# Kernel tuning notes

Hardware: AMD Instinct MI355X
Metric: run time of the kernel (lower is better)

## Reference

```python
import jax, jax.numpy as jnp
import numpy as np

N_DISEASES = 8192
N_MIRNAS = 16384
N_TOTAL = N_DISEASES + N_MIRNAS
D = 256
B = 65536
K = 50
EPS = 1e-8


def setup_inputs() -> dict:
    key = jax.random.key(0)
    k1, k2, k3, k4, k5, k6 = jax.random.split(key, 6)
    h = jax.random.normal(k1, (N_TOTAL, D), dtype=jnp.float32)
    emb = jax.random.normal(k2, (N_TOTAL, D), dtype=jnp.float32)
    src_init = jax.random.normal(k3, (B, D), dtype=jnp.float32)
    dst_init = jax.random.normal(k4, (B, D), dtype=jnp.float32)
    diseases = jax.random.randint(k5, (B,), 0, N_DISEASES, dtype=jnp.int32)
    mirnas = jax.random.randint(k6, (B,), N_DISEASES, N_TOTAL, dtype=jnp.int32)
    return {"h": h, "emb": emb, "src_init": src_init, "dst_init": dst_init,
            "diseases": diseases, "mirnas": mirnas}


def _cos(a, b):
    # cosine similarity along the last axis, eps-clamped like torch's F.cosine_similarity
    na = jnp.maximum(jnp.linalg.norm(a, axis=-1), EPS)
    nb = jnp.maximum(jnp.linalg.norm(b, axis=-1), EPS)
    return jnp.sum(a * b, axis=-1) / (na * nb)


def _pair_contrastive(pos_sim, neg_sim):
    # -log(exp(pos) / (exp(pos) + exp(neg))) = logaddexp(0, neg - pos)
    return jnp.mean(jnp.logaddexp(jnp.float32(0.0), neg_sim - pos_sim))


def _knn_feature_update(features, k):
    # [N, N] dense similarity, top-(k+1), drop self, gather + mean
    sim = features @ features.T                      # [N, N]
    _, idx = jax.lax.top_k(sim, k + 1)               # [N, k+1]
    idx = idx[:, 1:]                                 # drop self-match
    nbr = features[idx]                              # [N, k, D]
    return jnp.mean(nbr, axis=1)                     # [N, D]


def _knn_contrastive(feat_a, feat_b):
    center_a = jnp.mean(feat_a, axis=0)
    center_b = jnp.mean(feat_b, axis=0)
    sa_a = _cos(feat_a, center_a[None, :])
    sb_a = _cos(feat_a, center_b[None, :])
    loss_a = _pair_contrastive(sa_a, sb_a)
    sb_b = _cos(feat_b, center_b[None, :])
    sa_b = _cos(feat_b, center_a[None, :])
    loss_b = _pair_contrastive(sb_b, sa_b)
    return (loss_a + loss_b) * jnp.float32(0.5)


def reference(h, emb, src_init, dst_init, diseases, mirnas):
    h_d = h[diseases]                                # [B, D]
    h_m = h[mirnas]                                  # [B, D]
    pos_sim = _cos(h_d, src_init)
    neg_sim = _cos(h_d, dst_init)
    contrastive_loss = _pair_contrastive(pos_sim, neg_sim)

    upd_d = _knn_feature_update(emb[:N_DISEASES], K)
    upd_m = _knn_feature_update(emb[N_DISEASES:], K)
    feature_contrastive_loss = _knn_contrastive(upd_d, upd_m)

    # interactionPredictor modeled as sigmoid dot-product scorer
    scores = jax.nn.sigmoid(jnp.sum(h_d * h_m, axis=-1))  # [B]
    return scores, contrastive_loss, feature_contrastive_loss
```

## Files before the change

kernel.cpp:

```cpp
#include <hip/hip_runtime.h>
#include <math.h>

#define NDIS 8192
#define NMIR 16384
#define NTOT 24576
#define DIMD 256
#define BPAIR 65536
#define KSEL 50
#define EPSF 1e-8f
#define CBC 32
#define CAP 80
#define PSTR 320
#define ZD 2.066f
#define ZM 2.418f
#define ZFD 0.9035f
#define ZFM 1.331f
#define NKB 768

typedef __attribute__((ext_vector_type(8))) short bf16x8;
typedef __attribute__((ext_vector_type(4))) float f32x4;
typedef unsigned long long ull;

__device__ __forceinline__ float wredsum(float v) {
#pragma unroll
  for (int off = 1; off < 64; off <<= 1) v += __shfl_xor(v, off, 64);
  return v;
}

__device__ __forceinline__ int wredsumi(int v) {
#pragma unroll
  for (int off = 1; off < 64; off <<= 1) v += __shfl_xor(v, off, 64);
  return v;
}

__device__ __forceinline__ float softplusf(float x) {
  return fmaxf(x, 0.0f) + log1pf(expf(-fabsf(x)));
}

__device__ __forceinline__ float dot4f(const float4 a, const float4 b) {
  return a.x * b.x + a.y * b.y + a.z * b.z + a.w * b.w;
}

__device__ __forceinline__ unsigned short f2bf(float f) {
  unsigned u = __float_as_uint(f);
  unsigned r = (u + 0x7fffu + ((u >> 16) & 1u)) >> 16;
  return (unsigned short)r;
}

__device__ __forceinline__ float b2f(unsigned short x) {
  return __uint_as_float((unsigned)x << 16);
}

__device__ __forceinline__ unsigned ordu(float f) {
  unsigned u = __float_as_uint(f);
  return (u & 0x80000000u) ? ~u : (u | 0x80000000u);
}

__global__ __launch_bounds__(256) void convert_kernel(
    const float* __restrict__ in, unsigned short* __restrict__ out) {
  const int i = (blockIdx.x * 256 + threadIdx.x) * 4;
  const float4 v = *(const float4*)(in + i);
  ushort4 o;
  o.x = f2bf(v.x); o.y = f2bf(v.y); o.z = f2bf(v.z); o.w = f2bf(v.w);
  *(ushort4*)(out + i) = o;
}

__global__ __launch_bounds__(256) void colsum_kernel(
    const unsigned short* __restrict__ embb, float* __restrict__ colpart) {
  const int d = threadIdx.x;
  const int r0 = blockIdx.x * 256;
  float s = 0.0f;
  for (int i = 0; i < 256; ++i) s += b2f(embb[(size_t)(r0 + i) * DIMD + d]);
  colpart[blockIdx.x * DIMD + d] = s;
}

__global__ __launch_bounds__(256) void tau_kernel(
    const unsigned short* __restrict__ embb, const float* __restrict__ colpart,
    float* __restrict__ tau, float2* __restrict__ musig,
    unsigned* __restrict__ cnts, unsigned* __restrict__ flags) {
  __shared__ float cm[DIMD];
  const int lane = threadIdx.x & 63;
  const int widx = threadIdx.x >> 6;
  const bool bism = blockIdx.x >= 32;
  {
    const int b0 = bism ? 32 : 0, b1 = bism ? 96 : 32;
    const float Ninv = 1.0f / (bism ? (float)NMIR : (float)NDIS);
    float s = 0.0f;
    for (int b = b0; b < b1; ++b) s += colpart[b * DIMD + threadIdx.x];
    cm[threadIdx.x] = s * Ninv;
  }
  __syncthreads();
  const int r0 = blockIdx.x * 256 + widx * 64;
  const float z = bism ? ZM : ZD;
  for (int rr = 0; rr < 64; ++rr) {
    const int row = r0 + rr;
    const float4 cmv = ((const float4*)cm)[lane];
    const ushort4 u = ((const ushort4*)(embb + (size_t)row * DIMD))[lane];
    const float fx = b2f(u.x), fy = b2f(u.y), fz = b2f(u.z), fw = b2f(u.w);
    float dot = fx * cmv.x + fy * cmv.y + fz * cmv.z + fw * cmv.w;
    float nsq = fx * fx + fy * fy + fz * fz + fw * fw;
    dot = wredsum(dot);
    nsq = wredsum(nsq);
    const float sig = sqrtf(nsq);
    if (lane == 0) {
      tau[row] = dot + z * sig;
      musig[row] = make_float2(dot, sig);
      flags[row] = 0u;
    }
    if (lane < 4) cnts[row * 4 + lane] = 0u;
  }
}

__global__ __launch_bounds__(256, 3) void knn_kernel(
    const unsigned short* __restrict__ embb, const float* __restrict__ tau,
    unsigned* __restrict__ part, unsigned* __restrict__ cnts,
    unsigned* __restrict__ flags, const float* __restrict__ h,
    const float* __restrict__ srci, const float* __restrict__ dsti,
    const int* __restrict__ dis, const int* __restrict__ mir,
    float* __restrict__ scores, float* __restrict__ pairpart) {
  __shared__ char lds[3][CBC * 512];
  __shared__ float wsum[4];

  const int tid = threadIdx.x;
  const int lane = tid & 63;
  const int widx = tid >> 6;
  const int q4 = lane >> 4;
  const int l15 = lane & 15;
  const int sh16 = q4 * 16;
  const unsigned lmask = (1u << l15) - 1u;

  const int bid = blockIdx.x;
  const bool ism = bid < 512;
  const int rt = ism ? (bid >> 2) : ((bid - 512) >> 2);
  const int strip = ism ? (bid & 3) : ((bid - 512) & 3);
  const int sw = ism ? 4096 : 2048;
  const int nch = sw / CBC;
  const int gbase = ism ? NDIS : 0;
  const unsigned short* fb = embb + (size_t)gbase * DIMD;

  const int rowbase = rt * 128 + widx * 32;
  const int colstart = strip * sw;
  const char* gb = (const char*)fb;

  bf16x8 afr[2][8];
#pragma unroll
  for (int rg = 0; rg < 2; ++rg) {
    const int arow = rowbase + rg * 16 + l15;
    const char* ab = (const char*)fb + (size_t)arow * 512 + q4 * 16;
#pragma unroll
    for (int kk = 0; kk < 8; ++kk)
      afr[rg][kk] = *(const bf16x8*)(ab + (size_t)kk * 64);
  }

  float tau8[2][4];
  unsigned offb[2];
  int cnt8[2][4];
#pragma unroll
  for (int rg = 0; rg < 2; ++rg) {
    const int db = rowbase + rg * 16 + q4 * 4;
    offb[rg] = (unsigned)(gbase + db) * PSTR + strip * CAP;
#pragma unroll
    for (int j = 0; j < 4; ++j) {
      tau8[rg][j] = tau[gbase + db + j];
      cnt8[rg][j] = 0;
    }
  }

  auto stage = [&](char* dst, int cb0n) {
#pragma unroll
    for (int it = 0; it < 4; ++it) {
      const int m = widx * 4 + it;
      const int col = m * 2 + (lane >> 5);
      const int qq = (lane & 31) * 16;
      const int koff = qq ^ ((col & 7) << 4);
      const char* src = gb + (size_t)(colstart + cb0n + col) * 512 + koff;
      __builtin_amdgcn_global_load_lds(
          (const __attribute__((address_space(1))) void*)src,
          (__attribute__((address_space(3))) void*)(dst + m * 1024), 16, 0, 0);
    }
  };

  char* b0 = lds[0];
  char* b1 = lds[1];
  char* b2 = lds[2];
  stage(b0, 0);
  stage(b1, CBC);
  for (int ch = 0; ch < nch; ++ch) {
    if (ch < nch - 1)
      asm volatile("s_waitcnt vmcnt(4)" ::: "memory");
    else
      asm volatile("s_waitcnt vmcnt(0)" ::: "memory");
    __builtin_amdgcn_sched_barrier(0);
    __builtin_amdgcn_s_barrier();
    __builtin_amdgcn_sched_barrier(0);
    if (ch + 2 < nch) stage(b2, (ch + 2) * CBC);

    const char* bch = b0;
    const int cb0 = ch * CBC;
    f32x4 acc[2][2];
#pragma unroll
    for (int rg = 0; rg < 2; ++rg)
#pragma unroll
      for (int t = 0; t < 2; ++t) acc[rg][t] = (f32x4){0.f, 0.f, 0.f, 0.f};

#pragma unroll
    for (int t = 0; t < 2; ++t) {
      const int col = t * 16 + l15;
      const char* bbase = bch + (size_t)col * 512;
      const int xr = (col & 7) << 4;
#pragma unroll
      for (int kk = 0; kk < 8; ++kk) {
        const int koff = (kk * 64 + (q4 * 16)) ^ xr;
        const bf16x8 b = *(const bf16x8*)(bbase + koff);
        acc[0][t] = __builtin_amdgcn_mfma_f32_16x16x32_bf16(afr[0][kk], b,
                                                            acc[0][t], 0, 0, 0);
        acc[1][t] = __builtin_amdgcn_mfma_f32_16x16x32_bf16(afr[1][kk], b,
                                                            acc[1][t], 0, 0, 0);
      }
    }

#pragma unroll
    for (int t = 0; t < 2; ++t) {
      const int colb = colstart + cb0 + t * 16;
      const unsigned kc = (unsigned)(16383 - (colb + l15));
#pragma unroll
      for (int rg = 0; rg < 2; ++rg) {
        const bool dchr = (colb == rowbase + rg * 16);
#pragma unroll
        for (int j = 0; j < 4; ++j) {
          const float v = acc[rg][t][j];
          bool ok = v > tau8[rg][j];
          if (dchr) ok = ok && (l15 != (q4 * 4 + j));
          const ull m = __ballot(ok);
          if (m) {
            const unsigned m16 = (unsigned)(m >> sh16) & 0xFFFFu;
            const int rank = __popc(m16 & lmask);
            const int slot = cnt8[rg][j] + rank;
            if (ok && slot < CAP)
              part[offb[rg] + (unsigned)(j * PSTR) + slot] =
                  ((ordu(v) >> 14) << 14) | kc;
            cnt8[rg][j] += __popc(m16);
          }
        }
      }
    }

    char* tp = b0; b0 = b1; b1 = b2; b2 = tp;
  }

#pragma unroll
  for (int rg = 0; rg < 2; ++rg) {
#pragma unroll
    for (int j = 0; j < 4; ++j) {
      if (l15 == 0) {
        const int growg = gbase + rowbase + rg * 16 + q4 * 4 + j;
        const int c = cnt8[rg][j];
        cnts[growg * 4 + strip] = (unsigned)(c < CAP ? c : CAP);
        if (c > CAP) flags[growg] = 1u;
      }
    }
  }

  const int gw = bid * 4 + widx;
  float lsum = 0.0f;
  for (int b = gw; b < BPAIR; b += NKB * 4) {
    const int d = dis[b];
    const int m = mir[b];
    const float4 a4 = ((const float4*)(h + (size_t)d * DIMD))[lane];
    const float4 m4 = ((const float4*)(h + (size_t)m * DIMD))[lane];
    const float4 s4 = ((const float4*)(srci + (size_t)b * DIMD))[lane];
    const float4 t4 = ((const float4*)(dsti + (size_t)b * DIMD))[lane];
    float aa = dot4f(a4, a4);
    float ss = dot4f(s4, s4);
    float tt = dot4f(t4, t4);
    float as = dot4f(a4, s4);
    float at = dot4f(a4, t4);
    float am = dot4f(a4, m4);
    aa = wredsum(aa); ss = wredsum(ss); tt = wredsum(tt);
    as = wredsum(as); at = wredsum(at); am = wredsum(am);
    const float ra = fmaxf(sqrtf(aa), EPSF);
    const float pos = as / (ra * fmaxf(sqrtf(ss), EPSF));
    const float neg = at / (ra * fmaxf(sqrtf(tt), EPSF));
    lsum += softplusf(neg - pos);
    if (lane == 0) scores[b] = 1.0f / (1.0f + expf(-am));
  }
  if (lane == 0) wsum[widx] = lsum;
  __syncthreads();
  if (tid == 0)
    pairpart[bid] = (wsum[0] + wsum[1]) + (wsum[2] + wsum[3]);
}

__global__ __launch_bounds__(256) void fallback_kernel(
    const unsigned short* __restrict__ embb, const float2* __restrict__ musig,
    unsigned* __restrict__ part, unsigned* __restrict__ cnts,
    const unsigned* __restrict__ flags, unsigned* __restrict__ fbbuf) {
  __shared__ unsigned short frow[4][DIMD];
  const int lane = threadIdx.x & 63;
  const int widx = threadIdx.x >> 6;
  const int wid = blockIdx.x * 4 + widx;
  const ull bel = (1ull << lane) - 1ull;

  for (int row = wid * 96; row < wid * 96 + 96; ++row) {
    unsigned tot = 0;
    for (int s = 0; s < 4; ++s) tot += cnts[row * 4 + s];
    if (!(flags[row] || tot < KSEL)) continue;

    const bool ism = row >= NDIS;
    const int lrow = ism ? row - NDIS : row;
    const int Ng = ism ? NMIR : NDIS;
    const unsigned short* fb = embb + (ism ? (size_t)NDIS * DIMD : 0);
    const float2 ms = musig[row];
    const float tp = ms.x + (ism ? ZFM : ZFD) * ms.y;

    ((ushort4*)frow[widx])[lane] =
        ((const ushort4*)(fb + (size_t)lrow * DIMD))[lane];

    unsigned* fk = fbbuf + (size_t)wid * 4096;
    int fc = 0;
    for (int cb = 0; cb < Ng; cb += 64) {
      const int col = cb + lane;
      float s = 0.0f;
      for (int d0 = 0; d0 < DIMD; d0 += 4) {
        const ushort4 uc = *(const ushort4*)(fb + (size_t)col * DIMD + d0);
        const ushort4 ur = *(const ushort4*)(&frow[widx][d0]);
        s += b2f(uc.x) * b2f(ur.x) + b2f(uc.y) * b2f(ur.y) +
             b2f(uc.z) * b2f(ur.z) + b2f(uc.w) * b2f(ur.w);
      }
      const bool a = (s > tp) && (col != lrow);
      const ull m = __ballot(a);
      const int sl = fc + __popcll(m & bel);
      if (a && sl < 4096) fk[sl] = ((ordu(s) >> 14) << 14) | (16383u - col);
      fc += __popcll(m);
    }
    if (fc > 4096) fc = 4096;

    unsigned lo = 0u, hi = 0xFFFFFFFFu;
    for (int it = 0; it < 32; ++it) {
      const unsigned mid = lo + ((hi - lo) >> 1);
      int c = 0;
      for (int i = lane; i < fc; i += 64) c += (fk[i] > mid) ? 1 : 0;
      c = wredsumi(c);
      if (c >= KSEL) lo = mid; else hi = mid;
    }
    int wc = 0;
    for (int base = 0; base < fc; base += 64) {
      const int i = base + lane;
      const bool w = (i < fc) && (fk[i] > lo);
      const ull m = __ballot(w);
      const int pos = wc + __popcll(m & bel);
      if (w) part[(size_t)row * PSTR + pos] = fk[i];
      wc += __popcll(m);
    }
    if (lane < 4) cnts[row * 4 + lane] = (lane == 0) ? KSEL : 0u;
  }
}

__global__ __launch_bounds__(256) void merge_kernel(
    const unsigned short* __restrict__ embb, const unsigned* __restrict__ part,
    const unsigned* __restrict__ cnts, float* __restrict__ upd_d,
    float* __restrict__ upd_m) {
  __shared__ unsigned kb[4][PSTR];
  const int lane = threadIdx.x & 63;
  const int widx = threadIdx.x >> 6;
  const int row = blockIdx.x * 4 + widx;
  const bool ism = row >= NDIS;
  const int lrow = ism ? row - NDIS : row;
  const unsigned short* fe = embb + (ism ? (size_t)NDIS * DIMD : 0);
  float* upd =
      (ism ? upd_m + (size_t)lrow * DIMD : upd_d + (size_t)lrow * DIMD);
  const ull bel = (1ull << lane) - 1ull;

  int T = 0;
  for (int s = 0; s < 4; ++s) {
    const int c = (int)cnts[row * 4 + s];
    for (int i = lane; i < c; i += 64)
      kb[widx][T + i] = part[(size_t)row * PSTR + s * CAP + i];
    T += c;
  }
  unsigned k[5];
#pragma unroll
  for (int i = 0; i < 5; ++i) {
    const int idx = i * 64 + lane;
    k[i] = (idx < T) ? kb[widx][idx] : 0u;
  }

  unsigned lo = 0u, hi = 0xFFFFFFFFu;
  for (int it = 0; it < 32; ++it) {
    const unsigned mid = lo + ((hi - lo) >> 1);
    int c = 0;
#pragma unroll
    for (int i = 0; i < 5; ++i) c += __popcll(__ballot(k[i] > mid));
    if (c >= KSEL) lo = mid; else hi = mid;
  }
  int wc = 0;
#pragma unroll
  for (int i = 0; i < 5; ++i) {
    const bool w = k[i] > lo;
    const ull m = __ballot(w);
    const int pos = wc + __popcll(m & bel);
    if (w) kb[widx][pos] = 16383u - (k[i] & 16383u);
    wc += __popcll(m);
  }

  float ax = 0.f, ay = 0.f, az = 0.f, aw = 0.f;
#pragma unroll 10
  for (int t = 0; t < KSEL; ++t) {
    const int col = (int)kb[widx][t];
    const ushort4 u = ((const ushort4*)(fe + (size_t)col * DIMD))[lane];
    ax += b2f(u.x); ay += b2f(u.y); az += b2f(u.z); aw += b2f(u.w);
  }
  const float inv = 1.0f / (float)KSEL;
  float4 o;
  o.x = ax * inv; o.y = ay * inv; o.z = az * inv; o.w = aw * inv;
  ((float4*)upd)[lane] = o;
}

__global__ __launch_bounds__(256) void center_partial(
    const float* __restrict__ upd, float* __restrict__ part) {
  const int c = threadIdx.x;
  const int r0 = blockIdx.x * 128;
  float s = 0.0f;
  for (int i = 0; i < 128; ++i) s += upd[(size_t)(r0 + i) * DIMD + c];
  part[blockIdx.x * DIMD + c] = s;
}

__global__ __launch_bounds__(256) void center_final(
    const float* __restrict__ part, float* __restrict__ center,
    float* __restrict__ cnorm) {
  const int g = blockIdx.x;
  const int c = threadIdx.x;
  const int b0 = g ? 64 : 0, b1 = g ? 192 : 64;
  const float N = g ? (float)NMIR : (float)NDIS;
  float s = 0.0f;
  for (int b = b0; b < b1; ++b) s += part[b * DIMD + c];
  s /= N;
  center[g * DIMD + c] = s;
  __shared__ float red[256];
  red[c] = s * s;
  __syncthreads();
  for (int off = 128; off > 0; off >>= 1) {
    if (c < off) red[c] += red[c + off];
    __syncthreads();
  }
  if (c == 0) cnorm[g] = sqrtf(red[0]);
}

__global__ __launch_bounds__(256) void knn_loss(
    const float* __restrict__ upd_d, const float* __restrict__ upd_m,
    const float* __restrict__ centers, const float* __restrict__ cnorms,
    float* __restrict__ lpa, float* __restrict__ lpb) {
  const int lane = threadIdx.x & 63;
  const int widx = threadIdx.x >> 6;
  const int bid = blockIdx.x;
  const bool ism = bid >= 128;
  const int lb = ism ? bid - 128 : bid;
  const int N = ism ? NMIR : NDIS;
  const int nw = ism ? 1024 : 512;
  const float* upd = ism ? upd_m : upd_d;
  const int gw = lb * 4 + widx;
  const float4 ca = ((const float4*)centers)[lane];
  const float4 cbv = ((const float4*)(centers + DIMD))[lane];
  const float na = fmaxf(cnorms[0], EPSF);
  const float nb = fmaxf(cnorms[1], EPSF);
  float lsum = 0.0f;
  for (int r = gw; r < N; r += nw) {
    const float4 u = ((const float4*)(upd + (size_t)r * DIMD))[lane];
    float uu = dot4f(u, u);
    float uca = dot4f(u, ca);
    float ucb = dot4f(u, cbv);
    uu = wredsum(uu); uca = wredsum(uca); ucb = wredsum(ucb);
    const float nu = fmaxf(sqrtf(uu), EPSF);
    const float sa = uca / (nu * na);
    const float sb = ucb / (nu * nb);
    const float x = ism ? (sa - sb) : (sb - sa);
    lsum += softplusf(x);
  }
  __shared__ float wsum[4];
  if (lane == 0) wsum[widx] = lsum;
  __syncthreads();
  if (threadIdx.x == 0) {
    const float v = (wsum[0] + wsum[1]) + (wsum[2] + wsum[3]);
    if (ism) lpb[lb] = v; else lpa[lb] = v;
  }
}

__global__ __launch_bounds__(256) void finalize_kernel(
    const float* __restrict__ pairpart, const float* __restrict__ lpa,
    const float* __restrict__ lpb, float* __restrict__ out) {
  __shared__ float red[256];
  const int t = threadIdx.x;

  float s = 0.0f;
  for (int i = t; i < NKB; i += 256) s += pairpart[i];
  red[t] = s;
  __syncthreads();
  for (int off = 128; off > 0; off >>= 1) {
    if (t < off) red[t] += red[t + off];
    __syncthreads();
  }
  const float pairsum = red[0];
  __syncthreads();

  red[t] = (t < 128) ? lpa[t] : 0.0f;
  __syncthreads();
  for (int off = 128; off > 0; off >>= 1) {
    if (t < off) red[t] += red[t + off];
    __syncthreads();
  }
  const float la = red[0];
  __syncthreads();

  red[t] = lpb[t];
  __syncthreads();
  for (int off = 128; off > 0; off >>= 1) {
    if (t < off) red[t] += red[t + off];
    __syncthreads();
  }
  const float lb = red[0];

  if (t == 0) {
    out[BPAIR] = pairsum / (float)BPAIR;
    out[BPAIR + 1] = 0.5f * (la / (float)NDIS + lb / (float)NMIR);
  }
}

extern "C" void kernel_launch(void* const* d_in, const int* in_sizes, int n_in,
                              void* d_out, int out_size, void* d_ws,
                              size_t ws_size, hipStream_t stream) {
  const float* h = (const float*)d_in[0];
  const float* emb = (const float*)d_in[1];
  const float* srci = (const float*)d_in[2];
  const float* dsti = (const float*)d_in[3];
  const int* dis = (const int*)d_in[4];
  const int* mir = (const int*)d_in[5];
  float* out = (float*)d_out;

  float* W = (float*)d_ws;
  float* upd_d = W;
  float* upd_m = upd_d + (size_t)NDIS * DIMD;
  float* pairpart = upd_m + (size_t)NMIR * DIMD;
  float* cpart = pairpart + 1024;
  float* centers = cpart + 192 * DIMD;
  float* cnorms = centers + 512;
  float* lpa = cnorms + 64;
  float* lpb = lpa + 128;
  float* colpart = lpb + 256;
  float* tau = colpart + 96 * DIMD;
  float2* musig = (float2*)(tau + NTOT);
  unsigned* flags = (unsigned*)(musig + NTOT);
  unsigned* cnts = flags + NTOT;
  unsigned short* embb = (unsigned short*)(cnts + NTOT * 4);
  unsigned* part = (unsigned*)(embb + (size_t)NTOT * DIMD);
  unsigned* fbbuf = part + (size_t)NTOT * PSTR;

  convert_kernel<<<(NTOT * DIMD) / 1024, 256, 0, stream>>>(emb, embb);
  colsum_kernel<<<96, 256, 0, stream>>>(embb, colpart);
  tau_kernel<<<96, 256, 0, stream>>>(embb, colpart, tau, musig, cnts, flags);
  knn_kernel<<<NKB, 256, 0, stream>>>(embb, tau, part, cnts, flags, h, srci,
                                      dsti, dis, mir, out, pairpart);
  fallback_kernel<<<64, 256, 0, stream>>>(embb, musig, part, cnts, flags,
                                          fbbuf);
  merge_kernel<<<NTOT / 4, 256, 0, stream>>>(embb, part, cnts, upd_d, upd_m);
  center_partial<<<192, 256, 0, stream>>>(upd_d, cpart);
  center_final<<<2, 256, 0, stream>>>(cpart, centers, cnorms);
  knn_loss<<<384, 256, 0, stream>>>(upd_d, upd_m, centers, cnorms, lpa, lpb);
  finalize_kernel<<<1, 256, 0, stream>>>(pairpart, lpa, lpb, out);
}
```

Before: 488.7 us.

## Use 512-thread kNN blocks with 8 column strips and fuse convert with colsum

Each kNN block now has 8 waves covering 256 rows, and the column range is split into 8 narrower strips. The per-strip candidate capacity drops to 48, and overflowing candidates are written into the last slot instead of being dropped. The merge kernel skips empty ballot rounds. The fp32-to-bf16 conversion is fused with the column-sum pass, so the bf16 buffer is no longer reread. The fused convert kernel runs only 96 blocks, which may leave bandwidth unused, and the smaller capacity may send more rows to the fallback path.

```diff
diff --git a/kernel.cpp b/kernel.cpp
--- a/kernel.cpp
+++ b/kernel.cpp
@@ -9,8 +9,9 @@
 #define KSEL 50
 #define EPSF 1e-8f
 #define CBC 32
-#define CAP 80
-#define PSTR 320
+#define CAP 48
+#define NSTR 8
+#define PSTR 384
 #define ZD 2.066f
 #define ZM 2.418f
 #define ZFD 0.9035f
@@ -56,21 +57,18 @@
   return (u & 0x80000000u) ? ~u : (u | 0x80000000u);
 }
 
-__global__ __launch_bounds__(256) void convert_kernel(
-    const float* __restrict__ in, unsigned short* __restrict__ out) {
-  const int i = (blockIdx.x * 256 + threadIdx.x) * 4;
-  const float4 v = *(const float4*)(in + i);
-  ushort4 o;
-  o.x = f2bf(v.x); o.y = f2bf(v.y); o.z = f2bf(v.z); o.w = f2bf(v.w);
-  *(ushort4*)(out + i) = o;
-}
-
-__global__ __launch_bounds__(256) void colsum_kernel(
-    const unsigned short* __restrict__ embb, float* __restrict__ colpart) {
+__global__ __launch_bounds__(256) void convert_colsum_kernel(
+    const float* __restrict__ in, unsigned short* __restrict__ out,
+    float* __restrict__ colpart) {
   const int d = threadIdx.x;
   const int r0 = blockIdx.x * 256;
   float s = 0.0f;
-  for (int i = 0; i < 256; ++i) s += b2f(embb[(size_t)(r0 + i) * DIMD + d]);
+  for (int i = 0; i < 256; ++i) {
+    const float v = in[(size_t)(r0 + i) * DIMD + d];
+    const unsigned short b = f2bf(v);
+    out[(size_t)(r0 + i) * DIMD + d] = b;
+    s += b2f(b);
+  }
   colpart[blockIdx.x * DIMD + d] = s;
 }
 
@@ -107,11 +105,11 @@
       musig[row] = make_float2(dot, sig);
       flags[row] = 0u;
     }
-    if (lane < 4) cnts[row * 4 + lane] = 0u;
-  }
-}
-
-__global__ __launch_bounds__(256, 3) void knn_kernel(
+    if (lane < NSTR) cnts[row * NSTR + lane] = 0u;
+  }
+}
+
+__global__ __launch_bounds__(512, 6) void knn_kernel(
     const unsigned short* __restrict__ embb, const float* __restrict__ tau,
     unsigned* __restrict__ part, unsigned* __restrict__ cnts,
     unsigned* __restrict__ flags, const float* __restrict__ h,
@@ -119,7 +117,7 @@
     const int* __restrict__ dis, const int* __restrict__ mir,
     float* __restrict__ scores, float* __restrict__ pairpart) {
   __shared__ char lds[3][CBC * 512];
-  __shared__ float wsum[4];
+  __shared__ float wsum[8];
 
   const int tid = threadIdx.x;
   const int lane = tid & 63;
@@ -127,18 +125,20 @@
   const int q4 = lane >> 4;
   const int l15 = lane & 15;
   const int sh16 = q4 * 16;
-  const unsigned lmask = (1u << l15) - 1u;
+
+  const ull gmask64 = 0xFFFFull << sh16;
+  const ull bel16 = ((1ull << lane) - 1ull) & gmask64;
 
   const int bid = blockIdx.x;
   const bool ism = bid < 512;
-  const int rt = ism ? (bid >> 2) : ((bid - 512) >> 2);
-  const int strip = ism ? (bid & 3) : ((bid - 512) & 3);
-  const int sw = ism ? 4096 : 2048;
+  const int rt = ism ? (bid >> 3) : ((bid - 512) >> 3);
+  const int strip = ism ? (bid & 7) : ((bid - 512) & 7);
+  const int sw = ism ? 2048 : 1024;
   const int nch = sw / CBC;
   const int gbase = ism ? NDIS : 0;
   const unsigned short* fb = embb + (size_t)gbase * DIMD;
 
-  const int rowbase = rt * 128 + widx * 32;
+  const int rowbase = rt * 256 + widx * 32;
   const int colstart = strip * sw;
   const char* gb = (const char*)fb;
 
@@ -168,8 +168,8 @@
 
   auto stage = [&](char* dst, int cb0n) {
 #pragma unroll
-    for (int it = 0; it < 4; ++it) {
-      const int m = widx * 4 + it;
+    for (int it = 0; it < 2; ++it) {
+      const int m = widx * 2 + it;
       const int col = m * 2 + (lane >> 5);
       const int qq = (lane & 31) * 16;
       const int koff = qq ^ ((col & 7) << 4);
@@ -187,7 +187,7 @@
   stage(b1, CBC);
   for (int ch = 0; ch < nch; ++ch) {
     if (ch < nch - 1)
-      asm volatile("s_waitcnt vmcnt(4)" ::: "memory");
+      asm volatile("s_waitcnt vmcnt(2)" ::: "memory");
     else
       asm volatile("s_waitcnt vmcnt(0)" ::: "memory");
     __builtin_amdgcn_sched_barrier(0);
@@ -233,13 +233,13 @@
           if (dchr) ok = ok && (l15 != (q4 * 4 + j));
           const ull m = __ballot(ok);
           if (m) {
-            const unsigned m16 = (unsigned)(m >> sh16) & 0xFFFFu;
-            const int rank = __popc(m16 & lmask);
+            const int rank = __popcll(m & bel16);
             const int slot = cnt8[rg][j] + rank;
-            if (ok && slot < CAP)
-              part[offb[rg] + (unsigned)(j * PSTR) + slot] =
+            const int ss = slot < (CAP - 1) ? slot : (CAP - 1);
+            if (ok)
+              part[offb[rg] + (unsigned)(j * PSTR) + ss] =
                   ((ordu(v) >> 14) << 14) | kc;
-            cnt8[rg][j] += __popc(m16);
+            cnt8[rg][j] += (int)__popcll(m & gmask64);
           }
         }
       }
@@ -255,15 +255,15 @@
       if (l15 == 0) {
         const int growg = gbase + rowbase + rg * 16 + q4 * 4 + j;
         const int c = cnt8[rg][j];
-        cnts[growg * 4 + strip] = (unsigned)(c < CAP ? c : CAP);
-        if (c > CAP) flags[growg] = 1u;
+        cnts[growg * NSTR + strip] = (unsigned)(c < CAP ? c : CAP);
+        if (c > CAP - 1) flags[growg] = 1u;
       }
     }
   }
 
-  const int gw = bid * 4 + widx;
+  const int gw = bid * 8 + widx;
   float lsum = 0.0f;
-  for (int b = gw; b < BPAIR; b += NKB * 4) {
+  for (int b = gw; b < BPAIR; b += NKB * 8) {
     const int d = dis[b];
     const int m = mir[b];
     const float4 a4 = ((const float4*)(h + (size_t)d * DIMD))[lane];
@@ -286,8 +286,12 @@
   }
   if (lane == 0) wsum[widx] = lsum;
   __syncthreads();
-  if (tid == 0)
-    pairpart[bid] = (wsum[0] + wsum[1]) + (wsum[2] + wsum[3]);
+  if (tid == 0) {
+    float s = 0.0f;
+#pragma unroll
+    for (int w = 0; w < 8; ++w) s += wsum[w];
+    pairpart[bid] = s;
+  }
 }
 
 __global__ __launch_bounds__(256) void fallback_kernel(
@@ -302,7 +306,7 @@
 
   for (int row = wid * 96; row < wid * 96 + 96; ++row) {
     unsigned tot = 0;
-    for (int s = 0; s < 4; ++s) tot += cnts[row * 4 + s];
+    for (int s = 0; s < NSTR; ++s) tot += cnts[row * NSTR + s];
     if (!(flags[row] || tot < KSEL)) continue;
 
     const bool ism = row >= NDIS;
@@ -351,7 +355,7 @@
       if (w) part[(size_t)row * PSTR + pos] = fk[i];
       wc += __popcll(m);
     }
-    if (lane < 4) cnts[row * 4 + lane] = (lane == 0) ? KSEL : 0u;
+    if (lane < NSTR) cnts[row * NSTR + lane] = (lane == 0) ? KSEL : 0u;
   }
 }
 
@@ -371,15 +375,16 @@
   const ull bel = (1ull << lane) - 1ull;
 
   int T = 0;
-  for (int s = 0; s < 4; ++s) {
-    const int c = (int)cnts[row * 4 + s];
+  for (int s = 0; s < NSTR; ++s) {
+    const int c = (int)cnts[row * NSTR + s];
     for (int i = lane; i < c; i += 64)
       kb[widx][T + i] = part[(size_t)row * PSTR + s * CAP + i];
     T += c;
   }
-  unsigned k[5];
-#pragma unroll
-  for (int i = 0; i < 5; ++i) {
+  const int nr = (T + 63) >> 6;
+  unsigned k[6];
+#pragma unroll
+  for (int i = 0; i < 6; ++i) {
     const int idx = i * 64 + lane;
     k[i] = (idx < T) ? kb[widx][idx] : 0u;
   }
@@ -389,17 +394,20 @@
     const unsigned mid = lo + ((hi - lo) >> 1);
     int c = 0;
 #pragma unroll
-    for (int i = 0; i < 5; ++i) c += __popcll(__ballot(k[i] > mid));
+    for (int i = 0; i < 6; ++i)
+      if (i < nr) c += __popcll(__ballot(k[i] > mid));
     if (c >= KSEL) lo = mid; else hi = mid;
   }
   int wc = 0;
 #pragma unroll
-  for (int i = 0; i < 5; ++i) {
-    const bool w = k[i] > lo;
-    const ull m = __ballot(w);
-    const int pos = wc + __popcll(m & bel);
-    if (w) kb[widx][pos] = 16383u - (k[i] & 16383u);
-    wc += __popcll(m);
+  for (int i = 0; i < 6; ++i) {
+    if (i < nr) {
+      const bool w = k[i] > lo;
+      const ull m = __ballot(w);
+      const int pos = wc + __popcll(m & bel);
+      if (w) kb[widx][pos] = 16383u - (k[i] & 16383u);
+      wc += __popcll(m);
+    }
   }
 
   float ax = 0.f, ay = 0.f, az = 0.f, aw = 0.f;
@@ -549,14 +557,13 @@
   float2* musig = (float2*)(tau + NTOT);
   unsigned* flags = (unsigned*)(musig + NTOT);
   unsigned* cnts = flags + NTOT;
-  unsigned short* embb = (unsigned short*)(cnts + NTOT * 4);
+  unsigned short* embb = (unsigned short*)(cnts + NTOT * NSTR);
   unsigned* part = (unsigned*)(embb + (size_t)NTOT * DIMD);
   unsigned* fbbuf = part + (size_t)NTOT * PSTR;
 
-  convert_kernel<<<(NTOT * DIMD) / 1024, 256, 0, stream>>>(emb, embb);
-  colsum_kernel<<<96, 256, 0, stream>>>(embb, colpart);
+  convert_colsum_kernel<<<96, 256, 0, stream>>>(emb, embb, colpart);
   tau_kernel<<<96, 256, 0, stream>>>(embb, colpart, tau, musig, cnts, flags);
-  knn_kernel<<<NKB, 256, 0, stream>>>(embb, tau, part, cnts, flags, h, srci,
+  knn_kernel<<<NKB, 512, 0, stream>>>(embb, tau, part, cnts, flags, h, srci,
                                       dsti, dis, mir, out, pairpart);
   fallback_kernel<<<64, 256, 0, stream>>>(embb, musig, part, cnts, flags,
                                           fbbuf);
```

Result: slower. 1.728 ms (+253.7%).
